# Kernel tuning notes

Measured on AMD Instinct MI355X. Metric: run time of the kernel, lower is better.

The kernel has to match this reference:

```python
import jax, jax.numpy as jnp
import numpy as np

VOL_LO = np.array([-40.0, -40.0, -1.0], np.float32)
VOL_HI = np.array([40.0, 40.0, 5.4], np.float32)
VOXEL = 0.4
GRID = (200, 200, 16)  # ((hi-lo)/voxel).int() as in __init__
NUM_CLASSES = 18
EMPTY_LABEL = 17
K = 10  # static per-gaussian tile: 6*sigma_max/VOXEL + 1 <= 10 since sigma <= 0.5
EPS = 1e-6
N_GAUSS = 8192


def quat_to_rotmat(q):
    # wxyz quaternion -> rotation matrix (normalized, as in 3DGS)
    q = q / jnp.linalg.norm(q, axis=-1, keepdims=True)
    w, x, y, z = q[..., 0], q[..., 1], q[..., 2], q[..., 3]
    R = jnp.stack([
        1 - 2 * (y * y + z * z), 2 * (x * y - w * z), 2 * (x * z + w * y),
        2 * (x * y + w * z), 1 - 2 * (x * x + z * z), 2 * (y * z - w * x),
        2 * (x * z - w * y), 2 * (y * z + w * x), 1 - 2 * (x * x + y * y),
    ], axis=-1)
    return R.reshape(q.shape[:-1] + (3, 3))


def _grid_coords():
    H, W, D = GRID
    ii, jj, kk = jnp.meshgrid(jnp.arange(H), jnp.arange(W), jnp.arange(D), indexing='ij')
    g = jnp.stack([ii, jj, kk], axis=-1).astype(jnp.float32) + 0.5  # voxel centers
    return g * VOXEL + jnp.asarray(VOL_LO)


def setup_inputs() -> dict:
    key = jax.random.key(0)
    k1, k2, k3, k4, k5 = jax.random.split(key, 5)
    lo = jnp.asarray(VOL_LO)
    hi = jnp.asarray(VOL_HI)
    means3d = jax.random.uniform(k1, (N_GAUSS, 3)) * (hi - lo) + lo
    opacities = jax.random.uniform(k2, (N_GAUSS, 1))
    features = jax.random.normal(k3, (N_GAUSS, NUM_CLASSES - 1))
    scales = jax.random.uniform(k4, (N_GAUSS, 3)) * 0.4 + 0.1  # sigma in [0.1, 0.5]
    rotations = jax.random.normal(k5, (N_GAUSS, 4))
    empty_scalar = jnp.full((1,), 10.0, jnp.float32)
    return {"means3d": means3d, "opacities": opacities, "features": features,
            "scales": scales, "rotations": rotations, "empty_scalar": empty_scalar}


def reference(means3d, opacities, features, scales, rotations, empty_scalar):
    H, W, D = GRID
    lo = jnp.asarray(VOL_LO)
    hi = jnp.asarray(VOL_HI)
    dims = jnp.array(GRID, jnp.int32)

    # covariances = (R diag(s)) (R diag(s))^T
    R = quat_to_rotmat(rotations)                 # [N,3,3]
    Lm = R * scales[:, None, :]
    cov = Lm @ jnp.swapaxes(Lm, -1, -2)           # [N,3,3]
    cov_inv = jnp.linalg.inv(cov)
    sig = jnp.sqrt(jnp.diagonal(cov, axis1=-2, axis2=-1))  # [N,3]

    # clamped 3-sigma bounds + skip test (strict, matching torch)
    b_lo = jnp.clip(means3d - 3.0 * sig, lo, hi)
    b_hi = jnp.clip(means3d + 3.0 * sig, lo, hi)
    valid = (((b_lo > lo) | (b_hi > lo)) & ((b_lo < hi) | (b_hi < hi))).all(-1)  # [N]
    i_lo = ((b_lo - lo) / VOXEL).astype(jnp.int32)
    i_hi = ((b_hi - lo) / VOXEL).astype(jnp.int32)

    # static KxKxK tile per gaussian, masked to the inclusive [i_lo, i_hi] slice
    o = jnp.arange(K, dtype=jnp.int32)
    oi, oj, ok = jnp.meshgrid(o, o, o, indexing='ij')
    offs = jnp.stack([oi, oj, ok], -1).reshape(-1, 3)          # [K3,3]
    vox = i_lo[:, None, :] + offs[None]                        # [N,K3,3]
    mask = (vox <= i_hi[:, None, :]).all(-1) & (vox < dims).all(-1) & valid[:, None]

    coords = (vox.astype(jnp.float32) + 0.5) * VOXEL + lo      # voxel centers
    diff = coords - means3d[:, None, :]                        # [N,K3,3]
    maha = jnp.einsum('nki,nij,nkj->nk', diff, cov_inv, diff)  # [N,K3]
    dens = jnp.where(mask, opacities * jnp.exp(-0.5 * maha), 0.0)

    flat = jnp.where(mask, vox[..., 0] * (W * D) + vox[..., 1] * D + vox[..., 2], 0)

    feat18 = jnp.concatenate([features, jnp.zeros_like(features[:, :1])], -1)  # [N,18]
    gd = jnp.zeros((H * W * D,), jnp.float32).at[flat.reshape(-1)].add(dens.reshape(-1))
    gf = jnp.zeros((H * W * D, NUM_CLASSES), jnp.float32).at[flat.reshape(-1)].add(
        (dens[..., None] * feat18[:, None, :]).reshape(-1, NUM_CLASSES))

    # appended 'empty' gaussian spans the full grid -> splat densely
    gc = _grid_coords()                                        # [H,W,D,3]
    e_mean = (lo + hi) / 2.0
    e_range = hi - lo
    e_inv = jnp.diag(1.0 / (e_range ** 2))
    de = gc - e_mean
    maha_e = jnp.einsum('hwdi,ij,hwdj->hwd', de, e_inv, de)
    dens_e = jnp.exp(-0.5 * maha_e)                            # empty opacity = 1
    e_feat = jnp.zeros((NUM_CLASSES,), jnp.float32).at[EMPTY_LABEL].add(empty_scalar[0])

    grid_density = gd.reshape(H, W, D) + dens_e
    grid_feats = gf.reshape(H, W, D, NUM_CLASSES) + dens_e[..., None] * e_feat
    grid_feats = grid_feats / jnp.maximum(grid_density[..., None], EPS)
    return grid_density[..., None], grid_feats
```

## Files before the change

kernel.cpp:

```cpp
#include <hip/hip_runtime.h>

namespace {
constexpr int GH = 200, GW = 200, GD = 16;
constexpr int NV = GH * GW * GD;
constexpr int NCLS = 18;
constexpr int NF = 17;
constexpr int NG = 8192;
constexpr int KMAX = 10;
constexpr float VOX = 0.4f;
constexpr float LO0 = -40.f, LO1 = -40.f, LO2 = -1.f;
constexpr float HI0 = 40.f, HI1 = 40.f, HI2 = 5.4f;
constexpr float EPSV = 1e-6f;

constexpr int TILE_XY = 4;
constexpr int NTX = GH / TILE_XY;
constexpr int NTY = GW / TILE_XY;
constexpr int NT = NTX * NTY;
constexpr int REC_DW = 32;
constexpr int REC_V4 = REC_DW / 4;
constexpr int CAP = 1024;
constexpr int CH = 32;

constexpr float NHL2E = -0.72134752044448170368f;
}

__global__ __launch_bounds__(256) void gv_bin(
    const float* __restrict__ means,
    const float* __restrict__ opac,
    const float* __restrict__ feats,
    const float* __restrict__ scales,
    const float* __restrict__ rots,
    float* __restrict__ recs,
    int* __restrict__ counts,
    int* __restrict__ lists)
{
    const int g = blockIdx.x * blockDim.x + threadIdx.x;
    if (g >= NG) return;

    const float mx = means[g * 3 + 0];
    const float my = means[g * 3 + 1];
    const float mz = means[g * 3 + 2];
    const float sx = scales[g * 3 + 0];
    const float sy = scales[g * 3 + 1];
    const float sz = scales[g * 3 + 2];
    float qw = rots[g * 4 + 0];
    float qx = rots[g * 4 + 1];
    float qy = rots[g * 4 + 2];
    float qz = rots[g * 4 + 3];

    const float qn = rsqrtf(qw * qw + qx * qx + qy * qy + qz * qz);
    qw *= qn; qx *= qn; qy *= qn; qz *= qn;
    const float r00 = 1.f - 2.f * (qy * qy + qz * qz);
    const float r01 = 2.f * (qx * qy - qw * qz);
    const float r02 = 2.f * (qx * qz + qw * qy);
    const float r10 = 2.f * (qx * qy + qw * qz);
    const float r11 = 1.f - 2.f * (qx * qx + qz * qz);
    const float r12 = 2.f * (qy * qz - qw * qx);
    const float r20 = 2.f * (qx * qz - qw * qy);
    const float r21 = 2.f * (qy * qz + qw * qx);
    const float r22 = 1.f - 2.f * (qx * qx + qy * qy);

    const float s0 = sx * sx, s1 = sy * sy, s2 = sz * sz;
    const float c00 = r00 * r00 * s0 + r01 * r01 * s1 + r02 * r02 * s2;
    const float c11 = r10 * r10 * s0 + r11 * r11 * s1 + r12 * r12 * s2;
    const float c22 = r20 * r20 * s0 + r21 * r21 * s1 + r22 * r22 * s2;
    const float i0 = 1.f / s0, i1 = 1.f / s1, i2 = 1.f / s2;
    const float a00 = r00 * r00 * i0 + r01 * r01 * i1 + r02 * r02 * i2;
    const float a01 = r00 * r10 * i0 + r01 * r11 * i1 + r02 * r12 * i2;
    const float a02 = r00 * r20 * i0 + r01 * r21 * i1 + r02 * r22 * i2;
    const float a11 = r10 * r10 * i0 + r11 * r11 * i1 + r12 * r12 * i2;
    const float a12 = r10 * r20 * i0 + r11 * r21 * i1 + r12 * r22 * i2;
    const float a22 = r20 * r20 * i0 + r21 * r21 * i1 + r22 * r22 * i2;

    const float m3[3] = { mx, my, mz };
    const float sg[3] = { sqrtf(c00), sqrtf(c11), sqrtf(c22) };
    const float lo3[3] = { LO0, LO1, LO2 };
    const float hi3[3] = { HI0, HI1, HI2 };
    const int dims[3] = { GH, GW, GD };

    int il[3], sp[3];
    bool valid = true;
#pragma unroll
    for (int ax = 0; ax < 3; ++ax) {
        const float bl = fminf(fmaxf(m3[ax] - 3.f * sg[ax], lo3[ax]), hi3[ax]);
        const float bh = fminf(fmaxf(m3[ax] + 3.f * sg[ax], lo3[ax]), hi3[ax]);
        valid = valid &&
                (((bl > lo3[ax]) || (bh > lo3[ax])) && ((bl < hi3[ax]) || (bh < hi3[ax])));
        const int a = (int)((bl - lo3[ax]) / VOX);
        const int b = (int)((bh - lo3[ax]) / VOX);
        int s = b - a + 1;
        s = min(s, KMAX);
        s = min(s, dims[ax] - a);
        s = max(s, 0);
        il[ax] = a;
        sp[ax] = s;
    }

    const bool live = valid && sp[0] > 0 && sp[1] > 0 && sp[2] > 0;
    const int pack = live ? (sp[0] | (sp[1] << 8) | (sp[2] << 16)) : 0;

    float4* R4 = (float4*)(recs + (size_t)g * REC_DW);
    const float* F = feats + (size_t)g * NF;
    R4[0] = make_float4(mx, my, mz, opac[g]);
    R4[1] = make_float4(NHL2E * a00, NHL2E * a11, NHL2E * a22, 2.f * NHL2E * a01);
    R4[2] = make_float4(2.f * NHL2E * a02, 2.f * NHL2E * a12, F[0], F[1]);
    R4[3] = make_float4(F[2], F[3], F[4], F[5]);
    R4[4] = make_float4(F[6], F[7], F[8], F[9]);
    R4[5] = make_float4(F[10], F[11], F[12], F[13]);
    R4[6] = make_float4(F[14], F[15], F[16], __int_as_float(il[0]));
    R4[7] = make_float4(__int_as_float(il[1]), __int_as_float(il[2]),
                        __int_as_float(pack), 0.f);

    if (!live) return;

    const int tx0 = il[0] / TILE_XY;
    const int tx1 = (il[0] + sp[0] - 1) / TILE_XY;
    const int ty0 = il[1] / TILE_XY;
    const int ty1 = (il[1] + sp[1] - 1) / TILE_XY;
    for (int tx = tx0; tx <= tx1; ++tx)
        for (int ty = ty0; ty <= ty1; ++ty) {
            const int tile = tx * NTY + ty;
            const int idx = atomicAdd(counts + tile, 1);
            if (idx < CAP) lists[(size_t)tile * CAP + idx] = g;
        }
}

__global__ __launch_bounds__(64) void gv_gather(
    const float* __restrict__ recs,
    const int* __restrict__ counts,
    const int* __restrict__ lists,
    const float* __restrict__ empty_scalar,
    float* __restrict__ out)
{
    __shared__ float4 s_rec[2][CH * REC_V4];

    const int tile = blockIdx.x;
    const int tx = tile / NTY;
    const int ty = tile - tx * NTY;

    const int lane = threadIdx.x;
    const int lx = lane >> 4;
    const int ly = (lane >> 2) & 3;
    const int vz0 = (lane & 3) << 2;

    const int vx = tx * TILE_XY + lx;
    const int vy = ty * TILE_XY + ly;
    const float cx = ((float)vx + 0.5f) * VOX + LO0;
    const float cy = ((float)vy + 0.5f) * VOX + LO1;

    const int n = min(counts[tile], CAP);
    const int* __restrict__ lst = lists + (size_t)tile * CAP;

    float accd[4] = { 0.f, 0.f, 0.f, 0.f };
    float accf[4][NF];
#pragma unroll
    for (int j = 0; j < 4; ++j)
#pragma unroll
        for (int c = 0; c < NF; ++c) accf[j][c] = 0.f;

    const int e_ld = lane >> 1;
    const int q_ld = lane & 1;
    float4 r0, r1, r2, r3;

    const int nchunk = (n + CH - 1) / CH;
    int buf = 0;

    if (nchunk > 0) {
        const int idx = e_ld;
        if (idx < n) {
            const float4* src = (const float4*)recs + (size_t)lst[idx] * REC_V4 + q_ld * 4;
            r0 = src[0]; r1 = src[1]; r2 = src[2]; r3 = src[3];
            float4* dst = &s_rec[0][e_ld * REC_V4 + q_ld * 4];
            dst[0] = r0; dst[1] = r1; dst[2] = r2; dst[3] = r3;
        }
    }
    __syncthreads();

    for (int c = 0; c < nchunk; ++c) {
        const int nidx = (c + 1) * CH + e_ld;
        const bool nact = (c + 1 < nchunk) && (nidx < n);
        if (nact) {
            const float4* src = (const float4*)recs + (size_t)lst[nidx] * REC_V4 + q_ld * 4;
            r0 = src[0]; r1 = src[1]; r2 = src[2]; r3 = src[3];
        }

        const int m = min(CH, n - c * CH);
        for (int e = 0; e < m; ++e) {
            const float4* E = &s_rec[buf][e * REC_V4];
            const float4 e0 = E[0], e1 = E[1], e2 = E[2], e3 = E[3];
            const float4 e4 = E[4], e5 = E[5], e6 = E[6], e7 = E[7];

            const int il0 = __float_as_int(e6.w);
            const int il1 = __float_as_int(e7.x);
            const int il2 = __float_as_int(e7.y);
            const int pk  = __float_as_int(e7.z);

            const bool inxy =
                ((unsigned)(vx - il0) < (unsigned)(pk & 255)) &
                ((unsigned)(vy - il1) < (unsigned)((pk >> 8) & 255));
            const unsigned spz = (unsigned)((pk >> 16) & 255);

            const float dx = cx - e0.x;
            const float dy = cy - e0.y;
            const float q0 = e1.x * dx * dx + e1.y * dy * dy + e1.w * dx * dy;
            const float q1 = e2.x * dx + e2.y * dy;
            const float A22 = e1.z;
            const float op = e0.w, mzv = e0.z;

            const float f[NF] = { e2.z, e2.w, e3.x, e3.y, e3.z, e3.w,
                                  e4.x, e4.y, e4.z, e4.w,
                                  e5.x, e5.y, e5.z, e5.w,
                                  e6.x, e6.y, e6.z };

#pragma unroll
            for (int j = 0; j < 4; ++j) {
                const float cz = ((float)(vz0 + j) + 0.5f) * VOX + LO2;
                const float dz = cz - mzv;
                const float ee = q0 + dz * (q1 + A22 * dz);
                const bool in = inxy & ((unsigned)(vz0 + j - il2) < spz);
                const float dens = op * exp2f(ee);
                if (in) {
                    accd[j] += dens;
#pragma unroll
                    for (int cc = 0; cc < NF; ++cc) accf[j][cc] += dens * f[cc];
                }
            }
        }

        if (nact) {
            float4* dst = &s_rec[buf ^ 1][e_ld * REC_V4 + q_ld * 4];
            dst[0] = r0; dst[1] = r1; dst[2] = r2; dst[3] = r3;
        }
        __syncthreads();
        buf ^= 1;
    }

    const float es = empty_scalar[0];
    const float ex = (cx - 0.5f * (LO0 + HI0)) / (HI0 - LO0);
    const float ey = (cy - 0.5f * (LO1 + HI1)) / (HI1 - LO1);
    const float exy = ex * ex + ey * ey;

    float dsv[4], dev[4];
#pragma unroll
    for (int j = 0; j < 4; ++j) {
        const float cz = ((float)(vz0 + j) + 0.5f) * VOX + LO2;
        const float ez = (cz - 0.5f * (LO2 + HI2)) / (HI2 - LO2);
        dev[j] = __expf(-0.5f * (exy + ez * ez));
        dsv[j] = accd[j] + dev[j];
    }

    const int vbase = (vx * GW + vy) * GD + vz0;
    *(float4*)(out + vbase) = make_float4(dsv[0], dsv[1], dsv[2], dsv[3]);

#pragma unroll
    for (int j = 0; j < 4; ++j) {
        const float inv = 1.f / fmaxf(dsv[j], EPSV);
        float vals[NCLS];
#pragma unroll
        for (int c = 0; c < NF; ++c) vals[c] = accf[j][c] * inv;
        vals[NF] = dev[j] * es * inv;
        float2* of2 = (float2*)(out + NV + (size_t)(vbase + j) * NCLS);
#pragma unroll
        for (int p = 0; p < NCLS / 2; ++p)
            of2[p] = make_float2(vals[2 * p], vals[2 * p + 1]);
    }
}

extern "C" void kernel_launch(void* const* d_in, const int* in_sizes, int n_in,
                              void* d_out, int out_size, void* d_ws, size_t ws_size,
                              hipStream_t stream) {
    const float* means  = (const float*)d_in[0];
    const float* opac   = (const float*)d_in[1];
    const float* feats  = (const float*)d_in[2];
    const float* scales = (const float*)d_in[3];
    const float* rots   = (const float*)d_in[4];
    const float* esc    = (const float*)d_in[5];

    float* recs   = (float*)d_ws;
    int*   counts = (int*)(recs + (size_t)NG * REC_DW);
    int*   lists  = counts + ((NT + 63) & ~63);

    hipMemsetAsync(counts, 0, sizeof(int) * ((NT + 63) & ~63), stream);

    gv_bin<<<NG / 256, 256, 0, stream>>>(means, opac, feats, scales, rots,
                                         recs, counts, lists);
    gv_gather<<<NT, 64, 0, stream>>>(recs, counts, lists, esc, (float*)d_out);
}
```

Measured before the change: 105.4 us.

## Scatter full gaussian records into per-tile lists instead of index lists

The binning kernel now writes each gaussian's full 128-byte record directly into every tile bucket it overlaps, instead of a global record array plus per-tile index lists. The gather kernel then reads records contiguously from its tile's slab, with no indirect index load. Tile capacity drops from 1024 to 128 to bound the larger workspace, the bin block size shrinks to 64, and exp2f is replaced by the hardware exp2 builtin. The trade-offs are duplicated record writes in the bin kernel and silent truncation of any tile holding more than 128 gaussians.

```diff
diff --git a/kernel.cpp b/kernel.cpp
--- a/kernel.cpp
+++ b/kernel.cpp
@@ -18,21 +18,20 @@
 constexpr int NT = NTX * NTY;
 constexpr int REC_DW = 32;
 constexpr int REC_V4 = REC_DW / 4;
-constexpr int CAP = 1024;
+constexpr int CAP = 128;
 constexpr int CH = 32;
 
 constexpr float NHL2E = -0.72134752044448170368f;
 }
 
-__global__ __launch_bounds__(256) void gv_bin(
+__global__ __launch_bounds__(64) void gv_bin(
     const float* __restrict__ means,
     const float* __restrict__ opac,
     const float* __restrict__ feats,
     const float* __restrict__ scales,
     const float* __restrict__ rots,
-    float* __restrict__ recs,
     int* __restrict__ counts,
-    int* __restrict__ lists)
+    float4* __restrict__ lists)
 {
     const int g = blockIdx.x * blockDim.x + threadIdx.x;
     if (g >= NG) return;
@@ -96,22 +95,20 @@
         sp[ax] = s;
     }
 
-    const bool live = valid && sp[0] > 0 && sp[1] > 0 && sp[2] > 0;
-    const int pack = live ? (sp[0] | (sp[1] << 8) | (sp[2] << 16)) : 0;
-
-    float4* R4 = (float4*)(recs + (size_t)g * REC_DW);
+    if (!valid || sp[0] <= 0 || sp[1] <= 0 || sp[2] <= 0) return;
+    const int pack = sp[0] | (sp[1] << 8) | (sp[2] << 16);
+
     const float* F = feats + (size_t)g * NF;
-    R4[0] = make_float4(mx, my, mz, opac[g]);
-    R4[1] = make_float4(NHL2E * a00, NHL2E * a11, NHL2E * a22, 2.f * NHL2E * a01);
-    R4[2] = make_float4(2.f * NHL2E * a02, 2.f * NHL2E * a12, F[0], F[1]);
-    R4[3] = make_float4(F[2], F[3], F[4], F[5]);
-    R4[4] = make_float4(F[6], F[7], F[8], F[9]);
-    R4[5] = make_float4(F[10], F[11], F[12], F[13]);
-    R4[6] = make_float4(F[14], F[15], F[16], __int_as_float(il[0]));
-    R4[7] = make_float4(__int_as_float(il[1]), __int_as_float(il[2]),
-                        __int_as_float(pack), 0.f);
-
-    if (!live) return;
+    float4 R[REC_V4];
+    R[0] = make_float4(mx, my, mz, opac[g]);
+    R[1] = make_float4(NHL2E * a00, NHL2E * a11, NHL2E * a22, 2.f * NHL2E * a01);
+    R[2] = make_float4(2.f * NHL2E * a02, 2.f * NHL2E * a12, F[0], F[1]);
+    R[3] = make_float4(F[2], F[3], F[4], F[5]);
+    R[4] = make_float4(F[6], F[7], F[8], F[9]);
+    R[5] = make_float4(F[10], F[11], F[12], F[13]);
+    R[6] = make_float4(F[14], F[15], F[16], __int_as_float(il[0]));
+    R[7] = make_float4(__int_as_float(il[1]), __int_as_float(il[2]),
+                       __int_as_float(pack), 0.f);
 
     const int tx0 = il[0] / TILE_XY;
     const int tx1 = (il[0] + sp[0] - 1) / TILE_XY;
@@ -121,14 +118,17 @@
         for (int ty = ty0; ty <= ty1; ++ty) {
             const int tile = tx * NTY + ty;
             const int idx = atomicAdd(counts + tile, 1);
-            if (idx < CAP) lists[(size_t)tile * CAP + idx] = g;
+            if (idx < CAP) {
+                float4* dst = lists + ((size_t)tile * CAP + idx) * REC_V4;
+#pragma unroll
+                for (int u = 0; u < REC_V4; ++u) dst[u] = R[u];
+            }
         }
 }
 
 __global__ __launch_bounds__(64) void gv_gather(
-    const float* __restrict__ recs,
     const int* __restrict__ counts,
-    const int* __restrict__ lists,
+    const float4* __restrict__ lists,
     const float* __restrict__ empty_scalar,
     float* __restrict__ out)
 {
@@ -149,7 +149,7 @@
     const float cy = ((float)vy + 0.5f) * VOX + LO1;
 
     const int n = min(counts[tile], CAP);
-    const int* __restrict__ lst = lists + (size_t)tile * CAP;
+    const float4* __restrict__ tl = lists + (size_t)tile * CAP * REC_V4;
 
     float accd[4] = { 0.f, 0.f, 0.f, 0.f };
     float accf[4][NF];
@@ -165,14 +165,11 @@
     const int nchunk = (n + CH - 1) / CH;
     int buf = 0;
 
-    if (nchunk > 0) {
-        const int idx = e_ld;
-        if (idx < n) {
-            const float4* src = (const float4*)recs + (size_t)lst[idx] * REC_V4 + q_ld * 4;
-            r0 = src[0]; r1 = src[1]; r2 = src[2]; r3 = src[3];
-            float4* dst = &s_rec[0][e_ld * REC_V4 + q_ld * 4];
-            dst[0] = r0; dst[1] = r1; dst[2] = r2; dst[3] = r3;
-        }
+    if (nchunk > 0 && e_ld < n) {
+        const float4* src = tl + (size_t)e_ld * REC_V4 + q_ld * 4;
+        r0 = src[0]; r1 = src[1]; r2 = src[2]; r3 = src[3];
+        float4* dst = &s_rec[0][e_ld * REC_V4 + q_ld * 4];
+        dst[0] = r0; dst[1] = r1; dst[2] = r2; dst[3] = r3;
     }
     __syncthreads();
 
@@ -180,7 +177,7 @@
         const int nidx = (c + 1) * CH + e_ld;
         const bool nact = (c + 1 < nchunk) && (nidx < n);
         if (nact) {
-            const float4* src = (const float4*)recs + (size_t)lst[nidx] * REC_V4 + q_ld * 4;
+            const float4* src = tl + (size_t)nidx * REC_V4 + q_ld * 4;
             r0 = src[0]; r1 = src[1]; r2 = src[2]; r3 = src[3];
         }
 
@@ -218,7 +215,7 @@
                 const float dz = cz - mzv;
                 const float ee = q0 + dz * (q1 + A22 * dz);
                 const bool in = inxy & ((unsigned)(vz0 + j - il2) < spz);
-                const float dens = op * exp2f(ee);
+                const float dens = op * __builtin_amdgcn_exp2f(ee);
                 if (in) {
                     accd[j] += dens;
 #pragma unroll
@@ -276,13 +273,12 @@
     const float* rots   = (const float*)d_in[4];
     const float* esc    = (const float*)d_in[5];
 
-    float* recs   = (float*)d_ws;
-    int*   counts = (int*)(recs + (size_t)NG * REC_DW);
-    int*   lists  = counts + ((NT + 63) & ~63);
-
-    hipMemsetAsync(counts, 0, sizeof(int) * ((NT + 63) & ~63), stream);
-
-    gv_bin<<<NG / 256, 256, 0, stream>>>(means, opac, feats, scales, rots,
-                                         recs, counts, lists);
-    gv_gather<<<NT, 64, 0, stream>>>(recs, counts, lists, esc, (float*)d_out);
-}
+    int*    counts = (int*)d_ws;
+    float4* lists  = (float4*)((char*)d_ws + 64 * 1024);
+
+    hipMemsetAsync(counts, 0, sizeof(int) * NT, stream);
+
+    gv_bin<<<NG / 64, 64, 0, stream>>>(means, opac, feats, scales, rots,
+                                       counts, lists);
+    gv_gather<<<NT, 64, 0, stream>>>(counts, lists, esc, (float*)d_out);
+}
```

New measurement: 105.0 us. Within noise of the previous version (-0.4%).
